# Performance work log

Measured on AMD Instinct MI355X. Metric: run time of the kernel, lower is better.

Reference implementation:

```python
import jax, jax.numpy as jnp
import numpy as np

B, N, DEG = 128, 512, 16          # graphs, nodes/graph, avg degree
NB = B * N                        # 65536 nodes
E = NB * DEG                      # 1048576 edges
K1, K2, K3 = 410, 205, 103        # ceil(0.8*512), ceil(0.5*410), ceil(0.5*205)
H, C = 4, 32                      # GAT heads, head dim
F_IN, ED = 128, 7


def _glorot(key, shape, fan_in):
    return jax.random.normal(key, shape, dtype=jnp.float32) / np.float32(np.sqrt(fan_in))


def setup_inputs() -> dict:
    key = jax.random.key(0)
    ks = jax.random.split(key, 24)
    x = jax.random.normal(ks[0], (NB, F_IN), dtype=jnp.float32)
    # random intra-graph edges, then offset per graph
    src = jax.random.randint(ks[1], (E,), 0, N)
    dst = jax.random.randint(ks[2], (E,), 0, N)
    off = jnp.repeat(jnp.arange(B) * N, N * DEG)
    edge_index = jnp.stack([src + off, dst + off]).astype(jnp.int32)
    edge_attr = jax.random.normal(ks[3], (E, ED), dtype=jnp.float32)
    p = {
        'c1_wl': _glorot(ks[4], (F_IN, F_IN), F_IN), 'c1_bl': jnp.zeros((F_IN,), jnp.float32), 'c1_wr': _glorot(ks[5], (F_IN, F_IN), F_IN),
        'p1_w': _glorot(ks[6], (F_IN,), F_IN),
        'c2_wl': _glorot(ks[7], (F_IN, F_IN), F_IN), 'c2_bl': jnp.zeros((F_IN,), jnp.float32), 'c2_wr': _glorot(ks[8], (F_IN, F_IN), F_IN),
        'p2_wrel': _glorot(ks[9], (F_IN, 1), F_IN), 'p2_brel': jnp.zeros((1,), jnp.float32), 'p2_wroot': _glorot(ks[10], (F_IN, 1), F_IN),
        'g_w': _glorot(ks[11], (F_IN, H * C), F_IN), 'g_as': _glorot(ks[12], (H, C), C), 'g_ad': _glorot(ks[13], (H, C), C),
        'g_we': _glorot(ks[14], (ED, H * C), ED), 'g_ae': _glorot(ks[15], (H, C), C), 'g_b': jnp.zeros((H * C,), jnp.float32),
        'p3_wrel': _glorot(ks[16], (F_IN, 1), F_IN), 'p3_brel': jnp.zeros((1,), jnp.float32), 'p3_wroot': _glorot(ks[17], (F_IN, 1), F_IN),
        'l1_w': _glorot(ks[18], (F_IN, F_IN), F_IN), 'l1_b': jnp.zeros((F_IN,), jnp.float32),
        'l2_w': _glorot(ks[19], (F_IN, 64), F_IN), 'l2_b': jnp.zeros((64,), jnp.float32),
        'l3_w': _glorot(ks[20], (64, 1), 64), 'l3_b': jnp.zeros((1,), jnp.float32),
    }
    return {'x': x, 'edge_index': edge_index, 'edge_attr': edge_attr, **p}


def _sage(x, src, dst, emf, wl, bl, wr):
    # SAGEConv: mean-aggregate neighbors (masked edges), lin_l(agg)+lin_r(x)
    agg = jax.ops.segment_sum(x[src] * emf[:, None], dst, num_segments=NB)
    cnt = jax.ops.segment_sum(emf, dst, num_segments=NB)
    mean = agg / jnp.maximum(cnt, 1.0)[:, None]
    return mean @ wl + bl + x @ wr


def _graphconv(x, src, dst, emf, wrel, brel, wroot):
    # GraphConv (SAGPooling score GNN): add-aggregation
    agg = jax.ops.segment_sum(x[src] * emf[:, None], dst, num_segments=NB)
    return (agg @ wrel + brel + x @ wroot).reshape(-1)


def _pool(x, score, nmask, K):
    # per-graph static top-k (equal-size graphs) == PyG topk + filter
    masked = jnp.where(nmask, score, -jnp.inf).reshape(B, N)
    idx = jax.lax.top_k(masked, K)[1]
    nm = jnp.zeros((B, N), dtype=bool).at[jnp.arange(B)[:, None], idx].set(True).reshape(-1)
    x = jnp.where(nm[:, None], x * score[:, None], 0.0)
    return x, nm


def _gap(x, K):
    # global mean pool; dropped nodes are exactly zero, K live nodes per graph
    return x.reshape(B, N, F_IN).sum(axis=1) / K


def _gat(x, src, dst, emf, nmask, edge_attr, w, a_s, a_d, w_e, a_e, b):
    xs = (x @ w).reshape(NB, H, C)
    al_s = (xs * a_s).sum(-1)                                   # [NB,H]
    al_d = (xs * a_d).sum(-1)
    al_e = ((edge_attr @ w_e).reshape(E, H, C) * a_e).sum(-1)    # [E,H]
    alpha = jax.nn.leaky_relu(al_s[src] + al_d[dst] + al_e, 0.2)
    alpha = jnp.where(emf[:, None] > 0, alpha, -jnp.inf)
    # PyG add_self_loops=True with fill_value='mean' for edge_attr
    ea_mean = (edge_attr * emf[:, None]).sum(0) / jnp.maximum(emf.sum(), 1.0)
    al_se = ((ea_mean @ w_e).reshape(H, C) * a_e).sum(-1)        # [H]
    alpha_self = jax.nn.leaky_relu(al_s + al_d + al_se[None, :], 0.2)
    alpha_self = jnp.where(nmask[:, None], alpha_self, -jnp.inf)
    m = jnp.maximum(jax.ops.segment_max(alpha, dst, num_segments=NB), alpha_self)
    m = jnp.where(jnp.isfinite(m), m, 0.0)
    ex = jnp.exp(alpha - m[dst]) * emf[:, None]
    ex_s = jnp.where(nmask[:, None], jnp.exp(alpha_self - m), 0.0)
    den = jnp.maximum(jax.ops.segment_sum(ex, dst, num_segments=NB) + ex_s, 1e-16)
    num = jax.ops.segment_sum(ex[:, :, None] * xs[src], dst, num_segments=NB) + ex_s[:, :, None] * xs
    return (num / den[:, :, None]).reshape(NB, H * C) + b


def _forward(x, edge_index, edge_attr, c1_wl, c1_bl, c1_wr, p1_w, c2_wl, c2_bl, c2_wr,
             p2_wrel, p2_brel, p2_wroot, g_w, g_as, g_ad, g_we, g_ae, g_b,
             p3_wrel, p3_brel, p3_wroot, l1_w, l1_b, l2_w, l2_b, l3_w, l3_b):
    src, dst = edge_index[0], edge_index[1]
    nmask = jnp.ones((NB,), dtype=bool)
    emf = jnp.ones((E,), jnp.float32)

    # block 1: SAGEConv -> TopKPooling(0.8) -> gap
    x = jax.nn.relu(_sage(x, src, dst, emf, c1_wl, c1_bl, c1_wr))
    s1 = jnp.tanh((x @ p1_w) / jnp.linalg.norm(p1_w))
    x, nmask = _pool(x, s1, nmask, K1)
    emf = emf * nmask[src] * nmask[dst]
    x1 = _gap(x, K1)

    # block 2: SAGEConv -> SAGPooling(0.5) -> gap
    x = jax.nn.relu(_sage(x, src, dst, emf, c2_wl, c2_bl, c2_wr))
    s2 = jnp.tanh(_graphconv(x, src, dst, emf, p2_wrel, p2_brel, p2_wroot))
    x, nmask = _pool(x, s2, nmask, K2)
    emf = emf * nmask[src] * nmask[dst]
    x2 = _gap(x, K2)

    # block 3: GATConv(128->32x4, edge_dim=7) -> SAGPooling(0.5) -> gap
    x = jax.nn.relu(_gat(x, src, dst, emf, nmask, edge_attr, g_w, g_as, g_ad, g_we, g_ae, g_b))
    s3 = jnp.tanh(_graphconv(x, src, dst, emf, p3_wrel, p3_brel, p3_wroot))
    x, nmask = _pool(x, s3, nmask, K3)
    x3 = _gap(x, K3)

    h = x1 + x2 + x3
    h = jax.nn.relu(h @ l1_w + l1_b)
    h = jax.nn.relu(h @ l2_w + l2_b)   # dropout identity in eval
    return jax.nn.sigmoid(h @ l3_w + l3_b)[:, 0]


def reference(x, edge_index, edge_attr, c1_wl, c1_bl, c1_wr, p1_w, c2_wl, c2_bl, c2_wr,
              p2_wrel, p2_brel, p2_wroot, g_w, g_as, g_ad, g_we, g_ae, g_b,
              p3_wrel, p3_brel, p3_wroot, l1_w, l1_b, l2_w, l2_b, l3_w, l3_b):
    return _forward(x, edge_index, edge_attr, c1_wl, c1_bl, c1_wr, p1_w, c2_wl, c2_bl, c2_wr,
                    p2_wrel, p2_brel, p2_wroot, g_w, g_as, g_ad, g_we, g_ae, g_b,
                    p3_wrel, p3_brel, p3_wroot, l1_w, l1_b, l2_w, l2_b, l3_w, l3_b)
```

## Files before the change

kernel.cpp:

```cpp
#include <hip/hip_runtime.h>
#include <math.h>

#define NBV 65536
#define EV  1048576
#define BV  128
#define K1V 410
#define K2V 205
#define K3V 103
#define NL2 (BV*K2V)
#define NEG_BIG (-1.0e38f)

__device__ __forceinline__ float lrelu(float x){ return x > 0.f ? x : 0.2f*x; }

__global__ void k_sentinel(float* out, float v){
  int i = threadIdx.x;
  if (i < 128) out[i] = v;
}

__global__ void k_init1(float* nmask, int* dcnt){
  int i = blockIdx.x*blockDim.x + threadIdx.x;
  if (i < NBV) nmask[i] = 1.f;
  if (i < NBV+1) dcnt[i] = 0;
}

__global__ void k_zero_i(int* p, int n){
  int i = blockIdx.x*blockDim.x + threadIdx.x;
  if (i < n) p[i] = 0;
}

__global__ void k_hist(const int* dst, int* dcnt){
  int e = blockIdx.x*blockDim.x + threadIdx.x;
  if (e < EV) atomicAdd(&dcnt[dst[e]], 1);
}

__global__ void k_scan1(const int* dcnt, int* rp, int* bsum){
  __shared__ int sc[256];
  int t = threadIdx.x, i = blockIdx.x*256 + t;
  int v = dcnt[i];
  sc[t] = v; __syncthreads();
  for (int o = 1; o < 256; o <<= 1){
    int x = (t >= o) ? sc[t-o] : 0;
    __syncthreads();
    sc[t] += x;
    __syncthreads();
  }
  rp[i] = sc[t];
  if (t == 255) bsum[blockIdx.x] = sc[t];
}

__global__ void k_scan2(int* bsum){
  __shared__ int sc[256];
  int t = threadIdx.x;
  int v = bsum[t];
  sc[t] = v; __syncthreads();
  for (int o = 1; o < 256; o <<= 1){
    int x = (t >= o) ? sc[t-o] : 0;
    __syncthreads();
    sc[t] += x;
    __syncthreads();
  }
  bsum[t] = sc[t] - v;
}

__global__ void k_scan3(int* rp, const int* dcnt, const int* bsum){
  int t = threadIdx.x, i = blockIdx.x*256 + t;
  rp[i] = rp[i] - dcnt[i] + bsum[blockIdx.x];
  if (i == 0) rp[NBV] = EV;
}

__global__ void k_scatter(const int* src, const int* dst, const int* rp, int* fill,
                          int* csr_src, int* csr_eid){
  int e = blockIdx.x*blockDim.x + threadIdx.x;
  if (e < EV){
    int d = dst[e];
    int pos = atomicAdd(&fill[d], 1);
    int slot = rp[d] + pos;
    csr_src[slot] = src[e];
    csr_eid[slot] = e;
  }
}

__global__ void k_ve_inv(const float* g_we, const float* g_ae, const float* p1w, float* sml){
  __shared__ float sc[128];
  int t = threadIdx.x;
  if (t < 28){
    int ed = t >> 2, h = t & 3;
    float a = 0.f;
    for (int c = 0; c < 32; c++) a += g_we[ed*128 + h*32 + c] * g_ae[h*32 + c];
    sml[20 + t] = a;
  }
  float v = p1w[t];
  sc[t] = v*v; __syncthreads();
  for (int o = 64; o > 0; o >>= 1){ if (t < o) sc[t] += sc[t+o]; __syncthreads(); }
  if (t == 0) sml[0] = 1.f / sqrtf(sc[0]);
}

__global__ void k_ale(const float* ea, const float* ve, float* ALE){
  int e = blockIdx.x*blockDim.x + threadIdx.x;
  if (e < EV){
    float a0=0.f,a1=0.f,a2=0.f,a3=0.f;
    for (int ed = 0; ed < 7; ed++){
      float x = ea[e*7 + ed];
      a0 += x*ve[ed*4+0]; a1 += x*ve[ed*4+1]; a2 += x*ve[ed*4+2]; a3 += x*ve[ed*4+3];
    }
    float4 o; o.x=a0; o.y=a1; o.z=a2; o.w=a3;
    *(float4*)&ALE[(size_t)e*4] = o;
  }
}

__global__ void __launch_bounds__(256) k_sage_agg(const float* X, const float* nmask,
    const int* rp, const int* csr_src, float* AGG, int masked){
  int g = blockIdx.x & 127;
  int blk = blockIdx.x >> 7;
  int i = g*512 + blk*8 + (threadIdx.x >> 5);
  int c4 = threadIdx.x & 31;
  float ax=0.f,ay=0.f,az=0.f,aw=0.f,cnt=0.f;
  if (!masked || nmask[i] > 0.f){
    int r0 = rp[i], r1 = rp[i+1];
    int s = r0;
    for (; s + 4 <= r1; s += 4){
      int sn0 = csr_src[s+0], sn1 = csr_src[s+1], sn2 = csr_src[s+2], sn3 = csr_src[s+3];
      float nm0 = masked ? nmask[sn0] : 1.f;
      float nm1 = masked ? nmask[sn1] : 1.f;
      float nm2 = masked ? nmask[sn2] : 1.f;
      float nm3 = masked ? nmask[sn3] : 1.f;
      if (nm0 > 0.f){ float4 v = *(const float4*)&X[((size_t)sn0 << 7) + (c4 << 2)];
                      ax += v.x; ay += v.y; az += v.z; aw += v.w; cnt += 1.f; }
      if (nm1 > 0.f){ float4 v = *(const float4*)&X[((size_t)sn1 << 7) + (c4 << 2)];
                      ax += v.x; ay += v.y; az += v.z; aw += v.w; cnt += 1.f; }
      if (nm2 > 0.f){ float4 v = *(const float4*)&X[((size_t)sn2 << 7) + (c4 << 2)];
                      ax += v.x; ay += v.y; az += v.z; aw += v.w; cnt += 1.f; }
      if (nm3 > 0.f){ float4 v = *(const float4*)&X[((size_t)sn3 << 7) + (c4 << 2)];
                      ax += v.x; ay += v.y; az += v.z; aw += v.w; cnt += 1.f; }
    }
    for (; s < r1; s++){
      int sn = csr_src[s];
      float nm = masked ? nmask[sn] : 1.f;
      if (nm > 0.f){
        const float4 v = *(const float4*)&X[((size_t)sn << 7) + (c4 << 2)];
        ax += v.x; ay += v.y; az += v.z; aw += v.w; cnt += 1.f;
      }
    }
  }
  float inv = 1.f / fmaxf(cnt, 1.f);
  float4 o; o.x = ax*inv; o.y = ay*inv; o.z = az*inv; o.w = aw*inv;
  *(float4*)&AGG[((size_t)i << 7) + (c4 << 2)] = o;
}

__global__ void __launch_bounds__(512) k_gemm(const float* A1, const float* A2,
    const float* W1, const float* W2, const float* bias,
    float* OUT, int has2, int relu, int hasb,
    const int* ridx, int sc_mode,
    const float* sw1, const float* sw2, const float* sinv,
    float* so1, float* so2){
  __shared__ float ws[128][128];
  __shared__ float as[16][136];
  int t = threadIdx.x;
  int n0 = blockIdx.x * 128;
  int rowg = t >> 5;
  int colg = t & 31;
  int rb = rowg * 8;
  int jb = colg * 4;
  int an = t >> 2;
  int ak = (t & 3) << 2;
  int arow = ridx ? ridx[n0 + an] : (n0 + an);
  float acc[8][4];
  for (int r = 0; r < 8; r++)
    for (int j = 0; j < 4; j++) acc[r][j] = 0.f;
  int nmat = has2 ? 2 : 1;
  for (int m = 0; m < nmat; m++){
    const float* A = (m == 0) ? A1 : A2;
    const float* W = (m == 0) ? W1 : W2;
    __syncthreads();
    for (int ii = 0; ii < 8; ii++){
      int idx4 = t + 512*ii;
      int kk = idx4 >> 5;
      int jj = (idx4 & 31) << 2;
      *(float4*)&ws[kk][jj] = *(const float4*)&W[kk*128 + jj];
    }
    float4 rA = *(const float4*)&A[((size_t)arow << 7) + ak];
    for (int c = 0; c < 8; c++){
      if (c > 0) __syncthreads();
      as[ak+0][an] = rA.x;
      as[ak+1][an] = rA.y;
      as[ak+2][an] = rA.z;
      as[ak+3][an] = rA.w;
      __syncthreads();
      if (c+1 < 8)
        rA = *(const float4*)&A[((size_t)arow << 7) + (c+1)*16 + ak];
      int kb = c*16;
      for (int kk = 0; kk < 16; kk++){
        float4 wv = *(const float4*)&ws[kb+kk][jb];
        float4 aL = *(const float4*)&as[kk][rb];
        float4 aH = *(const float4*)&as[kk][rb+4];
        float a0=aL.x,a1=aL.y,a2=aL.z,a3=aL.w,a4=aH.x,a5=aH.y,a6=aH.z,a7=aH.w;
        acc[0][0]+=a0*wv.x; acc[0][1]+=a0*wv.y; acc[0][2]+=a0*wv.z; acc[0][3]+=a0*wv.w;
        acc[1][0]+=a1*wv.x; acc[1][1]+=a1*wv.y; acc[1][2]+=a1*wv.z; acc[1][3]+=a1*wv.w;
        acc[2][0]+=a2*wv.x; acc[2][1]+=a2*wv.y; acc[2][2]+=a2*wv.z; acc[2][3]+=a2*wv.w;
        acc[3][0]+=a3*wv.x; acc[3][1]+=a3*wv.y; acc[3][2]+=a3*wv.z; acc[3][3]+=a3*wv.w;
        acc[4][0]+=a4*wv.x; acc[4][1]+=a4*wv.y; acc[4][2]+=a4*wv.z; acc[4][3]+=a4*wv.w;
        acc[5][0]+=a5*wv.x; acc[5][1]+=a5*wv.y; acc[5][2]+=a5*wv.z; acc[5][3]+=a5*wv.w;
        acc[6][0]+=a6*wv.x; acc[6][1]+=a6*wv.y; acc[6][2]+=a6*wv.z; acc[6][3]+=a6*wv.w;
        acc[7][0]+=a7*wv.x; acc[7][1]+=a7*wv.y; acc[7][2]+=a7*wv.z; acc[7][3]+=a7*wv.w;
      }
    }
  }
  float bj0=0.f,bj1=0.f,bj2=0.f,bj3=0.f;
  if (hasb){
    bj0 = bias[jb+0]; bj1 = bias[jb+1]; bj2 = bias[jb+2]; bj3 = bias[jb+3];
  }
  int orow[8];
  for (int r = 0; r < 8; r++) orow[r] = ridx ? ridx[n0+rb+r] : (n0+rb+r);
  float w1x=0.f,w1y=0.f,w1z=0.f,w1w=0.f, w2x=0.f,w2y=0.f,w2z=0.f,w2w=0.f;
  if (sc_mode){
    float4 t1 = *(const float4*)&sw1[jb];
    w1x=t1.x; w1y=t1.y; w1z=t1.z; w1w=t1.w;
    if (sc_mode == 2){
      float4 t2 = *(const float4*)&sw2[jb];
      w2x=t2.x; w2y=t2.y; w2z=t2.z; w2w=t2.w;
    }
  }
  float pd1[8], pd2[8];
  for (int r = 0; r < 8; r++){
    float4 o;
    o.x = acc[r][0]+bj0; o.y = acc[r][1]+bj1; o.z = acc[r][2]+bj2; o.w = acc[r][3]+bj3;
    if (relu){
      o.x = fmaxf(o.x,0.f); o.y = fmaxf(o.y,0.f); o.z = fmaxf(o.z,0.f); o.w = fmaxf(o.w,0.f);
    }
    if (sc_mode){
      pd1[r] = o.x*w1x + o.y*w1y + o.z*w1z + o.w*w1w;
      if (sc_mode == 2) pd2[r] = o.x*w2x + o.y*w2y + o.z*w2z + o.w*w2w;
    }
    *(float4*)&OUT[((size_t)orow[r] << 7) + jb] = o;
  }
  if (sc_mode == 1){
    float inv = sinv[0];
    for (int r = 0; r < 8; r++){
      float a = pd1[r];
      for (int o = 16; o > 0; o >>= 1) a += __shfl_down(a, o, 32);
      if (colg == 0) so1[orow[r]] = tanhf(a * inv);
    }
  } else if (sc_mode == 2){
    for (int r = 0; r < 8; r++){
      float a = pd1[r];
      float b = pd2[r];
      for (int o = 16; o > 0; o >>= 1){
        a += __shfl_down(a, o, 32);
        b += __shfl_down(b, o, 32);
      }
      if (colg == 0){ so1[orow[r]] = a; so2[orow[r]] = b; }
    }
  }
}

__global__ void k_gconv(const float* q, const float* r, const float* nmask,
    const int* rp, const int* csr_src, const float* brel, float* s){
  int i = blockIdx.x*blockDim.x + threadIdx.x;
  if (i >= NBV) return;
  float acc = 0.f;
  if (nmask[i] > 0.f){
    int r0 = rp[i], r1 = rp[i+1];
    int t2 = r0;
    for (; t2 + 4 <= r1; t2 += 4){
      int sn0 = csr_src[t2+0], sn1 = csr_src[t2+1], sn2 = csr_src[t2+2], sn3 = csr_src[t2+3];
      float nm0 = nmask[sn0], nm1 = nmask[sn1], nm2 = nmask[sn2], nm3 = nmask[sn3];
      if (nm0 > 0.f) acc += q[sn0];
      if (nm1 > 0.f) acc += q[sn1];
      if (nm2 > 0.f) acc += q[sn2];
      if (nm3 > 0.f) acc += q[sn3];
    }
    for (; t2 < r1; t2++){
      int sn = csr_src[t2];
      if (nmask[sn] > 0.f) acc += q[sn];
    }
  }
  s[i] = tanhf(acc + brel[0] + r[i]);
}

__global__ void __launch_bounds__(512) k_pool(const float* s, float* nmask, float* sel,
                                              int K, int* cidx){
  __shared__ float sc[512];
  int b = blockIdx.x, t = threadIdx.x;
  int i = b*512 + t;
  float nm = nmask[i];
  float sv = s[i];
  float ms = (nm > 0.f) ? sv : NEG_BIG;
  sc[t] = ms;
  __syncthreads();
  int rank = 0;
  for (int j = 0; j < 512; j++){
    float o = sc[j];
    rank += ((o > ms) || (o == ms && j < t)) ? 1 : 0;
  }
  bool selb = rank < K;
  nmask[i] = selb ? 1.f : 0.f;
  sel[i] = selb ? sv : 0.f;
  if (cidx && selb) cidx[b*K + rank] = i;
}

__global__ void __launch_bounds__(128) k_scale_part(float* X, const float* sel, float* part){
  int b = blockIdx.x >> 3, q = blockIdx.x & 7, c = threadIdx.x;
  float acc = 0.f;
  for (int n = q*64; n < q*64 + 64; n++){
    int i = b*512 + n;
    float v = X[((size_t)i << 7) + c] * sel[i];
    X[((size_t)i << 7) + c] = v;
    acc += v;
  }
  part[(size_t)blockIdx.x*128 + c] = acc;
}

__global__ void __launch_bounds__(128) k_gap_final(const float* part, float* gap, float invK){
  int b = blockIdx.x, c = threadIdx.x;
  float s = 0.f;
  for (int q = 0; q < 8; q++) s += part[(size_t)(b*8+q)*128 + c];
  gap[b*128 + c] = s * invK;
}

__global__ void k_heads(const float* xs, const float* a_s, const float* a_d,
                        const int* cidx, int nlive4, float* alS, float* alD){
  int gid = blockIdx.x*blockDim.x + threadIdx.x;
  if (gid >= nlive4) return;
  int ii = gid >> 2, h = gid & 3;
  int i = cidx[ii];
  const float4* xr = (const float4*)&xs[((size_t)i << 7) + h*32];
  const float4* wa = (const float4*)&a_s[h*32];
  const float4* wd = (const float4*)&a_d[h*32];
  float as_ = 0.f, ad_ = 0.f;
  for (int c4 = 0; c4 < 8; c4++){
    float4 v = xr[c4]; float4 A = wa[c4]; float4 D = wd[c4];
    as_ += v.x*A.x + v.y*A.y + v.z*A.z + v.w*A.w;
    ad_ += v.x*D.x + v.y*D.y + v.z*D.z + v.w*D.w;
  }
  alS[i*4 + h] = as_; alD[i*4 + h] = ad_;
}

__global__ void __launch_bounds__(256) k_ea_part(const float* ea, const int* srcA, const int* dstA,
    const float* nmask, float* part){
  float p[8] = {0.f,0.f,0.f,0.f,0.f,0.f,0.f,0.f};
  for (int e = blockIdx.x*256 + threadIdx.x; e < EV; e += 256*256){
    if (nmask[srcA[e]] > 0.f && nmask[dstA[e]] > 0.f){
      for (int d = 0; d < 7; d++) p[d] += ea[e*7 + d];
      p[7] += 1.f;
    }
  }
  __shared__ float red[256];
  for (int comp = 0; comp < 8; comp++){
    red[threadIdx.x] = p[comp]; __syncthreads();
    for (int o = 128; o > 0; o >>= 1){ if (threadIdx.x < o) red[threadIdx.x] += red[threadIdx.x + o]; __syncthreads(); }
    if (threadIdx.x == 0) part[blockIdx.x*8 + comp] = red[0];
    __syncthreads();
  }
}

__global__ void k_ea_final(const float* part, float* easum){
  int h = threadIdx.x;
  if (h < 8){
    float s = 0.f;
    for (int b = 0; b < 256; b++) s += part[b*8 + h];
    easum[h] = s;
  }
}

__global__ void k_alse(const float* easum, const float* ve, float* alse){
  if (threadIdx.x == 0 && blockIdx.x == 0){
    float cnt = fmaxf(easum[7], 1.f);
    for (int h = 0; h < 4; h++){
      float s = 0.f;
      for (int ed = 0; ed < 7; ed++) s += (easum[ed]/cnt) * ve[ed*4 + h];
      alse[h] = s;
    }
  }
}

__global__ void __launch_bounds__(256) k_gat(const float* xs, const float* alS, const float* alD,
    const float* ALE, const float* nmask, const int* rp, const int* csr_src,
    const int* csr_eid, const float* alse, const float* g_b,
    const float* wrel, const float* wroot, float* qv, float* rv, float* OUT){
  int g = blockIdx.x & 127;
  int blk = blockIdx.x >> 7;
  int i = g*512 + blk*8 + (threadIdx.x >> 5);
  int lane = threadIdx.x & 31;
  int h = lane >> 3;
  int cidx = h*8 + (lane & 7);
  float nmi = nmask[i];
  const float4* xs4 = (const float4*)xs;
  float m = 0.f, den = 0.f;
  float4 acc; acc.x=0.f; acc.y=0.f; acc.z=0.f; acc.w=0.f;
  if (nmi > 0.f){
    float ald_i = alD[i*4 + h];
    m = lrelu(alS[i*4 + h] + ald_i + alse[h]);
    den = 1.f;
    acc = xs4[(size_t)i*32 + cidx];
    int r0 = rp[i], r1 = rp[i+1];
    int s = r0;
    for (; s + 4 <= r1; s += 4){
      int sn0 = csr_src[s+0], sn1 = csr_src[s+1], sn2 = csr_src[s+2], sn3 = csr_src[s+3];
      float nm0 = nmask[sn0], nm1 = nmask[sn1], nm2 = nmask[sn2], nm3 = nmask[sn3];
      if (nm0 > 0.f){
        float a = lrelu(alS[sn0*4 + h] + ald_i + ALE[(size_t)csr_eid[s+0]*4 + h]);
        float4 v = xs4[(size_t)sn0*32 + cidx];
        float mn = fmaxf(m, a); float pm = expf(m - mn); float pa = expf(a - mn);
        den = den*pm + pa;
        acc.x = acc.x*pm + pa*v.x; acc.y = acc.y*pm + pa*v.y;
        acc.z = acc.z*pm + pa*v.z; acc.w = acc.w*pm + pa*v.w;
        m = mn;
      }
      if (nm1 > 0.f){
        float a = lrelu(alS[sn1*4 + h] + ald_i + ALE[(size_t)csr_eid[s+1]*4 + h]);
        float4 v = xs4[(size_t)sn1*32 + cidx];
        float mn = fmaxf(m, a); float pm = expf(m - mn); float pa = expf(a - mn);
        den = den*pm + pa;
        acc.x = acc.x*pm + pa*v.x; acc.y = acc.y*pm + pa*v.y;
        acc.z = acc.z*pm + pa*v.z; acc.w = acc.w*pm + pa*v.w;
        m = mn;
      }
      if (nm2 > 0.f){
        float a = lrelu(alS[sn2*4 + h] + ald_i + ALE[(size_t)csr_eid[s+2]*4 + h]);
        float4 v = xs4[(size_t)sn2*32 + cidx];
        float mn = fmaxf(m, a); float pm = expf(m - mn); float pa = expf(a - mn);
        den = den*pm + pa;
        acc.x = acc.x*pm + pa*v.x; acc.y = acc.y*pm + pa*v.y;
        acc.z = acc.z*pm + pa*v.z; acc.w = acc.w*pm + pa*v.w;
        m = mn;
      }
      if (nm3 > 0.f){
        float a = lrelu(alS[sn3*4 + h] + ald_i + ALE[(size_t)csr_eid[s+3]*4 + h]);
        float4 v = xs4[(size_t)sn3*32 + cidx];
        float mn = fmaxf(m, a); float pm = expf(m - mn); float pa = expf(a - mn);
        den = den*pm + pa;
        acc.x = acc.x*pm + pa*v.x; acc.y = acc.y*pm + pa*v.y;
        acc.z = acc.z*pm + pa*v.z; acc.w = acc.w*pm + pa*v.w;
        m = mn;
      }
    }
    for (; s < r1; s++){
      int sn = csr_src[s];
      if (nmask[sn] > 0.f){
        float a = lrelu(alS[sn*4 + h] + ald_i + ALE[(size_t)csr_eid[s]*4 + h]);
        float4 v = xs4[(size_t)sn*32 + cidx];
        float mn = fmaxf(m, a); float pm = expf(m - mn); float pa = expf(a - mn);
        den = den*pm + pa;
        acc.x = acc.x*pm + pa*v.x; acc.y = acc.y*pm + pa*v.y;
        acc.z = acc.z*pm + pa*v.z; acc.w = acc.w*pm + pa*v.w;
        m = mn;
      }
    }
  }
  den = fmaxf(den, 1e-16f);
  float rd = 1.f/den;
  int cb = cidx << 2;
  float4 o;
  o.x = fmaxf(acc.x*rd + g_b[cb+0], 0.f);
  o.y = fmaxf(acc.y*rd + g_b[cb+1], 0.f);
  o.z = fmaxf(acc.z*rd + g_b[cb+2], 0.f);
  o.w = fmaxf(acc.w*rd + g_b[cb+3], 0.f);
  *(float4*)&OUT[((size_t)i << 7) + cb] = o;
  float4 wa = *(const float4*)&wrel[cb];
  float4 wb = *(const float4*)&wroot[cb];
  float aq = o.x*wa.x + o.y*wa.y + o.z*wa.z + o.w*wa.w;
  float ar = o.x*wb.x + o.y*wb.y + o.z*wb.z + o.w*wb.w;
  for (int off = 16; off > 0; off >>= 1){
    aq += __shfl_down(aq, off, 32);
    ar += __shfl_down(ar, off, 32);
  }
  if (lane == 0){ qv[i] = aq; rv[i] = ar; }
}

__global__ void __launch_bounds__(128) k_mlp(const float* x1g, const float* x2g, const float* x3g,
    const float* l1w, const float* l1b, const float* l2w, const float* l2b,
    const float* l3w, const float* l3b, float* out){
  __shared__ float hh[128];
  __shared__ float h2[128];
  __shared__ float h3[64];
  int b = blockIdx.x, t = threadIdx.x;
  hh[t] = x1g[b*128 + t] + x2g[b*128 + t] + x3g[b*128 + t];
  __syncthreads();
  float a = l1b[t];
  for (int k = 0; k < 128; k++) a += hh[k] * l1w[k*128 + t];
  h2[t] = fmaxf(a, 0.f);
  __syncthreads();
  if (t < 64){
    float a2 = l2b[t];
    for (int k = 0; k < 128; k++) a2 += h2[k] * l2w[k*64 + t];
    h3[t] = fmaxf(a2, 0.f);
  }
  __syncthreads();
  if (t == 0){
    float z = l3b[0];
    for (int k = 0; k < 64; k++) z += h3[k] * l3w[k];
    out[b] = 1.f/(1.f + expf(-z));
  }
}

extern "C" void kernel_launch(void* const* d_in, const int* in_sizes, int n_in,
                              void* d_out, int out_size, void* d_ws, size_t ws_size,
                              hipStream_t stream){
  const float* x       = (const float*)d_in[0];
  const int*   ei      = (const int*)d_in[1];
  const float* ea      = (const float*)d_in[2];
  const float* c1_wl   = (const float*)d_in[3];
  const float* c1_bl   = (const float*)d_in[4];
  const float* c1_wr   = (const float*)d_in[5];
  const float* p1_w    = (const float*)d_in[6];
  const float* c2_wl   = (const float*)d_in[7];
  const float* c2_bl   = (const float*)d_in[8];
  const float* c2_wr   = (const float*)d_in[9];
  const float* p2_wrel = (const float*)d_in[10];
  const float* p2_brel = (const float*)d_in[11];
  const float* p2_wroot= (const float*)d_in[12];
  const float* g_w     = (const float*)d_in[13];
  const float* g_as    = (const float*)d_in[14];
  const float* g_ad    = (const float*)d_in[15];
  const float* g_we    = (const float*)d_in[16];
  const float* g_ae    = (const float*)d_in[17];
  const float* g_b     = (const float*)d_in[18];
  const float* p3_wrel = (const float*)d_in[19];
  const float* p3_brel = (const float*)d_in[20];
  const float* p3_wroot= (const float*)d_in[21];
  const float* l1_w    = (const float*)d_in[22];
  const float* l1_b    = (const float*)d_in[23];
  const float* l2_w    = (const float*)d_in[24];
  const float* l2_b    = (const float*)d_in[25];
  const float* l3_w    = (const float*)d_in[26];
  const float* l3_b    = (const float*)d_in[27];
  float* out = (float*)d_out;
  (void)in_sizes; (void)n_in; (void)out_size;

  char* w = (char*)d_ws;
  size_t off = 0;
  float* AGG  = (float*)(w + off); off += (size_t)NBV*128*4;
  float* F1   = (float*)(w + off); off += (size_t)NBV*128*4;
  float* F2   = (float*)(w + off); off += (size_t)NBV*128*4;
  float* ALE  = (float*)(w + off); off += (size_t)EV*4*4;
  float* sA   = (float*)(w + off); off += (size_t)NBV*4;
  float* sel  = (float*)(w + off); off += (size_t)NBV*4;
  float* qv   = (float*)(w + off); off += (size_t)NBV*4;
  float* rv   = (float*)(w + off); off += (size_t)NBV*4;
  float* nmask= (float*)(w + off); off += (size_t)NBV*4;
  float* alS  = (float*)(w + off); off += (size_t)NBV*4*4;
  float* alD  = (float*)(w + off); off += (size_t)NBV*4*4;
  float* x1g  = (float*)(w + off); off += (size_t)BV*128*4;
  float* x2g  = (float*)(w + off); off += (size_t)BV*128*4;
  float* x3g  = (float*)(w + off); off += (size_t)BV*128*4;
  float* sml  = (float*)(w + off); off += 64*4;
  float* eprt = (float*)(w + off); off += 2048*4;
  float* gprt = (float*)(w + off); off += (size_t)1024*128*4;
  int* csr_src = (int*)(w + off); off += (size_t)EV*4;
  int* csr_eid = (int*)(w + off); off += (size_t)EV*4;
  int* rp      = (int*)(w + off); off += (size_t)(NBV+64)*4;
  int* dcnt    = (int*)(w + off); off += (size_t)(NBV+64)*4;
  int* cidx    = (int*)(w + off); off += (size_t)NBV*4;
  int* bsum    = (int*)(w + off); off += 1024;
  size_t needed = off;

  float sentinel = (ws_size >= needed) ? 0.125f : 0.875f;
  k_sentinel<<<1, 128, 0, stream>>>(out, sentinel);

  const int* srcA = ei;
  const int* dstA = ei + EV;

  k_init1<<<(NBV+256)/256, 256, 0, stream>>>(nmask, dcnt);
  k_hist<<<EV/256, 256, 0, stream>>>(dstA, dcnt);
  k_scan1<<<256, 256, 0, stream>>>(dcnt, rp, bsum);
  k_scan2<<<1, 256, 0, stream>>>(bsum);
  k_scan3<<<256, 256, 0, stream>>>(rp, dcnt, bsum);
  k_zero_i<<<(NBV+256)/256, 256, 0, stream>>>(dcnt, NBV+1);
  k_scatter<<<EV/256, 256, 0, stream>>>(srcA, dstA, rp, dcnt, csr_src, csr_eid);
  k_ve_inv<<<1, 128, 0, stream>>>(g_we, g_ae, p1_w, sml);
  k_ale<<<EV/256, 256, 0, stream>>>(ea, sml+20, ALE);

  k_sage_agg<<<(NBV*32)/256, 256, 0, stream>>>(x, nmask, rp, csr_src, AGG, 0);
  k_gemm<<<NBV/128, 512, 0, stream>>>(AGG, x, c1_wl, c1_wr, c1_bl, F1, 1, 1, 1,
                                      (const int*)nullptr, 1, p1_w, (const float*)nullptr, sml, sA, (float*)nullptr);
  k_pool<<<BV, 512, 0, stream>>>(sA, nmask, sel, K1V, (int*)nullptr);
  k_scale_part<<<BV*8, 128, 0, stream>>>(F1, sel, gprt);
  k_gap_final<<<BV, 128, 0, stream>>>(gprt, x1g, 1.f/(float)K1V);

  k_sage_agg<<<(NBV*32)/256, 256, 0, stream>>>(F1, nmask, rp, csr_src, AGG, 1);
  k_gemm<<<NBV/128, 512, 0, stream>>>(AGG, F1, c2_wl, c2_wr, c2_bl, F2, 1, 1, 1,
                                      (const int*)nullptr, 2, p2_wrel, p2_wroot, (const float*)nullptr, qv, rv);
  k_gconv<<<NBV/256, 256, 0, stream>>>(qv, rv, nmask, rp, csr_src, p2_brel, sA);
  k_pool<<<BV, 512, 0, stream>>>(sA, nmask, sel, K2V, cidx);
  k_scale_part<<<BV*8, 128, 0, stream>>>(F2, sel, gprt);
  k_gap_final<<<BV, 128, 0, stream>>>(gprt, x2g, 1.f/(float)K2V);

  k_gemm<<<NL2/128, 512, 0, stream>>>(F2, F2, g_w, g_w, g_b, AGG, 0, 0, 0,
                                      cidx, 0, (const float*)nullptr, (const float*)nullptr,
                                      (const float*)nullptr, (float*)nullptr, (float*)nullptr);
  k_heads<<<(NL2*4 + 255)/256, 256, 0, stream>>>(AGG, g_as, g_ad, cidx, NL2*4, alS, alD);
  k_ea_part<<<256, 256, 0, stream>>>(ea, srcA, dstA, nmask, eprt);
  k_ea_final<<<1, 64, 0, stream>>>(eprt, sml+8);
  k_alse<<<1, 64, 0, stream>>>(sml+8, sml+20, sml+16);
  k_gat<<<(NBV*32)/256, 256, 0, stream>>>(AGG, alS, alD, ALE, nmask, rp, csr_src, csr_eid,
                                          sml+16, g_b, p3_wrel, p3_wroot, qv, rv, F1);
  k_gconv<<<NBV/256, 256, 0, stream>>>(qv, rv, nmask, rp, csr_src, p3_brel, sA);
  k_pool<<<BV, 512, 0, stream>>>(sA, nmask, sel, K3V, (int*)nullptr);
  k_scale_part<<<BV*8, 128, 0, stream>>>(F1, sel, gprt);
  k_gap_final<<<BV, 128, 0, stream>>>(gprt, x3g, 1.f/(float)K3V);

  k_mlp<<<BV, 128, 0, stream>>>(x1g, x2g, x3g, l1_w, l1_b, l2_w, l2_b, l3_w, l3_b, out);
}
```

Measured before the change: 674.0 us.

## Compact pooled node lists to skip dead nodes in aggregation and GAT

After each pooling step the selected node indices are kept in per-pool index lists. The second SAGE aggregation and the GAT kernel now launch only over surviving nodes instead of all 512 per graph, and k_scale_part skips masked rows. The GEMM also stages the whole 128x128 A tile in shared memory at once, replacing the per-chunk double-sync loop. This roughly doubles the GEMM's LDS use, which can cut occupancy. The two tiny edge-attribute finalize kernels are merged into one. Rows for dead nodes are no longer rewritten, so the code relies on every later consumer masking them.

```diff
diff --git a/kernel.cpp b/kernel.cpp
--- a/kernel.cpp
+++ b/kernel.cpp
@@ -109,10 +109,14 @@
 }
 
 __global__ void __launch_bounds__(256) k_sage_agg(const float* X, const float* nmask,
-    const int* rp, const int* csr_src, float* AGG, int masked){
+    const int* rp, const int* csr_src, float* AGG, int masked,
+    const int* nidx, int kper){
   int g = blockIdx.x & 127;
   int blk = blockIdx.x >> 7;
-  int i = g*512 + blk*8 + (threadIdx.x >> 5);
+  int r = blk*8 + (threadIdx.x >> 5);
+  int i;
+  if (nidx){ if (r >= kper) return; i = nidx[g*kper + r]; }
+  else i = g*512 + r;
   int c4 = threadIdx.x & 31;
   float ax=0.f,ay=0.f,az=0.f,aw=0.f,cnt=0.f;
   if (!masked || nmask[i] > 0.f){
@@ -154,7 +158,7 @@
     const float* sw1, const float* sw2, const float* sinv,
     float* so1, float* so2){
   __shared__ float ws[128][128];
-  __shared__ float as[16][136];
+  __shared__ float as[128][136];
   int t = threadIdx.x;
   int n0 = blockIdx.x * 128;
   int rowg = t >> 5;
@@ -178,21 +182,20 @@
       int jj = (idx4 & 31) << 2;
       *(float4*)&ws[kk][jj] = *(const float4*)&W[kk*128 + jj];
     }
-    float4 rA = *(const float4*)&A[((size_t)arow << 7) + ak];
     for (int c = 0; c < 8; c++){
-      if (c > 0) __syncthreads();
-      as[ak+0][an] = rA.x;
-      as[ak+1][an] = rA.y;
-      as[ak+2][an] = rA.z;
-      as[ak+3][an] = rA.w;
-      __syncthreads();
-      if (c+1 < 8)
-        rA = *(const float4*)&A[((size_t)arow << 7) + (c+1)*16 + ak];
+      float4 rA = *(const float4*)&A[((size_t)arow << 7) + c*16 + ak];
+      as[c*16+ak+0][an] = rA.x;
+      as[c*16+ak+1][an] = rA.y;
+      as[c*16+ak+2][an] = rA.z;
+      as[c*16+ak+3][an] = rA.w;
+    }
+    __syncthreads();
+    for (int c = 0; c < 8; c++){
       int kb = c*16;
       for (int kk = 0; kk < 16; kk++){
         float4 wv = *(const float4*)&ws[kb+kk][jb];
-        float4 aL = *(const float4*)&as[kk][rb];
-        float4 aH = *(const float4*)&as[kk][rb+4];
+        float4 aL = *(const float4*)&as[kb+kk][rb];
+        float4 aH = *(const float4*)&as[kb+kk][rb+4];
         float a0=aL.x,a1=aL.y,a2=aL.z,a3=aL.w,a4=aH.x,a5=aH.y,a6=aH.z,a7=aH.w;
         acc[0][0]+=a0*wv.x; acc[0][1]+=a0*wv.y; acc[0][2]+=a0*wv.z; acc[0][3]+=a0*wv.w;
         acc[1][0]+=a1*wv.x; acc[1][1]+=a1*wv.y; acc[1][2]+=a1*wv.z; acc[1][3]+=a1*wv.w;
@@ -298,14 +301,17 @@
   if (cidx && selb) cidx[b*K + rank] = i;
 }
 
-__global__ void __launch_bounds__(128) k_scale_part(float* X, const float* sel, float* part){
+__global__ void __launch_bounds__(128) k_scale_part(float* X, const float* sel,
+    const float* nmask, float* part){
   int b = blockIdx.x >> 3, q = blockIdx.x & 7, c = threadIdx.x;
   float acc = 0.f;
   for (int n = q*64; n < q*64 + 64; n++){
     int i = b*512 + n;
-    float v = X[((size_t)i << 7) + c] * sel[i];
-    X[((size_t)i << 7) + c] = v;
-    acc += v;
+    if (nmask[i] > 0.f){
+      float v = X[((size_t)i << 7) + c] * sel[i];
+      X[((size_t)i << 7) + c] = v;
+      acc += v;
+    }
   }
   part[(size_t)blockIdx.x*128 + c] = acc;
 }
@@ -353,22 +359,21 @@
   }
 }
 
-__global__ void k_ea_final(const float* part, float* easum){
+__global__ void k_ea_fin(const float* part, const float* ve, float* alse){
+  __shared__ float es[8];
   int h = threadIdx.x;
   if (h < 8){
     float s = 0.f;
     for (int b = 0; b < 256; b++) s += part[b*8 + h];
-    easum[h] = s;
-  }
-}
-
-__global__ void k_alse(const float* easum, const float* ve, float* alse){
-  if (threadIdx.x == 0 && blockIdx.x == 0){
-    float cnt = fmaxf(easum[7], 1.f);
-    for (int h = 0; h < 4; h++){
+    es[h] = s;
+  }
+  __syncthreads();
+  if (h == 0){
+    float cnt = fmaxf(es[7], 1.f);
+    for (int hh = 0; hh < 4; hh++){
       float s = 0.f;
-      for (int ed = 0; ed < 7; ed++) s += (easum[ed]/cnt) * ve[ed*4 + h];
-      alse[h] = s;
+      for (int ed = 0; ed < 7; ed++) s += (es[ed]/cnt) * ve[ed*4 + hh];
+      alse[hh] = s;
     }
   }
 }
@@ -376,13 +381,17 @@
 __global__ void __launch_bounds__(256) k_gat(const float* xs, const float* alS, const float* alD,
     const float* ALE, const float* nmask, const int* rp, const int* csr_src,
     const int* csr_eid, const float* alse, const float* g_b,
-    const float* wrel, const float* wroot, float* qv, float* rv, float* OUT){
+    const float* wrel, const float* wroot, const int* nidx, int kper,
+    float* qv, float* rv, float* OUT){
   int g = blockIdx.x & 127;
   int blk = blockIdx.x >> 7;
-  int i = g*512 + blk*8 + (threadIdx.x >> 5);
+  int r = blk*8 + (threadIdx.x >> 5);
+  int i;
+  if (nidx){ if (r >= kper) return; i = nidx[g*kper + r]; }
+  else i = g*512 + r;
   int lane = threadIdx.x & 31;
   int h = lane >> 3;
-  int cidx = h*8 + (lane & 7);
+  int ch = h*8 + (lane & 7);
   float nmi = nmask[i];
   const float4* xs4 = (const float4*)xs;
   float m = 0.f, den = 0.f;
@@ -391,7 +400,7 @@
     float ald_i = alD[i*4 + h];
     m = lrelu(alS[i*4 + h] + ald_i + alse[h]);
     den = 1.f;
-    acc = xs4[(size_t)i*32 + cidx];
+    acc = xs4[(size_t)i*32 + ch];
     int r0 = rp[i], r1 = rp[i+1];
     int s = r0;
     for (; s + 4 <= r1; s += 4){
@@ -399,7 +408,7 @@
       float nm0 = nmask[sn0], nm1 = nmask[sn1], nm2 = nmask[sn2], nm3 = nmask[sn3];
       if (nm0 > 0.f){
         float a = lrelu(alS[sn0*4 + h] + ald_i + ALE[(size_t)csr_eid[s+0]*4 + h]);
-        float4 v = xs4[(size_t)sn0*32 + cidx];
+        float4 v = xs4[(size_t)sn0*32 + ch];
         float mn = fmaxf(m, a); float pm = expf(m - mn); float pa = expf(a - mn);
         den = den*pm + pa;
         acc.x = acc.x*pm + pa*v.x; acc.y = acc.y*pm + pa*v.y;
@@ -408,7 +417,7 @@
       }
       if (nm1 > 0.f){
         float a = lrelu(alS[sn1*4 + h] + ald_i + ALE[(size_t)csr_eid[s+1]*4 + h]);
-        float4 v = xs4[(size_t)sn1*32 + cidx];
+        float4 v = xs4[(size_t)sn1*32 + ch];
         float mn = fmaxf(m, a); float pm = expf(m - mn); float pa = expf(a - mn);
         den = den*pm + pa;
         acc.x = acc.x*pm + pa*v.x; acc.y = acc.y*pm + pa*v.y;
@@ -417,7 +426,7 @@
       }
       if (nm2 > 0.f){
         float a = lrelu(alS[sn2*4 + h] + ald_i + ALE[(size_t)csr_eid[s+2]*4 + h]);
-        float4 v = xs4[(size_t)sn2*32 + cidx];
+        float4 v = xs4[(size_t)sn2*32 + ch];
         float mn = fmaxf(m, a); float pm = expf(m - mn); float pa = expf(a - mn);
         den = den*pm + pa;
         acc.x = acc.x*pm + pa*v.x; acc.y = acc.y*pm + pa*v.y;
@@ -426,7 +435,7 @@
       }
       if (nm3 > 0.f){
         float a = lrelu(alS[sn3*4 + h] + ald_i + ALE[(size_t)csr_eid[s+3]*4 + h]);
-        float4 v = xs4[(size_t)sn3*32 + cidx];
+        float4 v = xs4[(size_t)sn3*32 + ch];
         float mn = fmaxf(m, a); float pm = expf(m - mn); float pa = expf(a - mn);
         den = den*pm + pa;
         acc.x = acc.x*pm + pa*v.x; acc.y = acc.y*pm + pa*v.y;
@@ -438,7 +447,7 @@
       int sn = csr_src[s];
       if (nmask[sn] > 0.f){
         float a = lrelu(alS[sn*4 + h] + ald_i + ALE[(size_t)csr_eid[s]*4 + h]);
-        float4 v = xs4[(size_t)sn*32 + cidx];
+        float4 v = xs4[(size_t)sn*32 + ch];
         float mn = fmaxf(m, a); float pm = expf(m - mn); float pa = expf(a - mn);
         den = den*pm + pa;
         acc.x = acc.x*pm + pa*v.x; acc.y = acc.y*pm + pa*v.y;
@@ -449,7 +458,7 @@
   }
   den = fmaxf(den, 1e-16f);
   float rd = 1.f/den;
-  int cb = cidx << 2;
+  int cb = ch << 2;
   float4 o;
   o.x = fmaxf(acc.x*rd + g_b[cb+0], 0.f);
   o.y = fmaxf(acc.y*rd + g_b[cb+1], 0.f);
@@ -550,7 +559,8 @@
   int* csr_eid = (int*)(w + off); off += (size_t)EV*4;
   int* rp      = (int*)(w + off); off += (size_t)(NBV+64)*4;
   int* dcnt    = (int*)(w + off); off += (size_t)(NBV+64)*4;
-  int* cidx    = (int*)(w + off); off += (size_t)NBV*4;
+  int* cidx1   = (int*)(w + off); off += (size_t)NBV*4;
+  int* cidx2   = (int*)(w + off); off += (size_t)NBV*4;
   int* bsum    = (int*)(w + off); off += 1024;
   size_t needed = off;
 
@@ -570,33 +580,33 @@
   k_ve_inv<<<1, 128, 0, stream>>>(g_we, g_ae, p1_w, sml);
   k_ale<<<EV/256, 256, 0, stream>>>(ea, sml+20, ALE);
 
-  k_sage_agg<<<(NBV*32)/256, 256, 0, stream>>>(x, nmask, rp, csr_src, AGG, 0);
+  k_sage_agg<<<(NBV*32)/256, 256, 0, stream>>>(x, nmask, rp, csr_src, AGG, 0,
+                                               (const int*)nullptr, 512);
   k_gemm<<<NBV/128, 512, 0, stream>>>(AGG, x, c1_wl, c1_wr, c1_bl, F1, 1, 1, 1,
                                       (const int*)nullptr, 1, p1_w, (const float*)nullptr, sml, sA, (float*)nullptr);
-  k_pool<<<BV, 512, 0, stream>>>(sA, nmask, sel, K1V, (int*)nullptr);
-  k_scale_part<<<BV*8, 128, 0, stream>>>(F1, sel, gprt);
+  k_pool<<<BV, 512, 0, stream>>>(sA, nmask, sel, K1V, cidx1);
+  k_scale_part<<<BV*8, 128, 0, stream>>>(F1, sel, nmask, gprt);
   k_gap_final<<<BV, 128, 0, stream>>>(gprt, x1g, 1.f/(float)K1V);
 
-  k_sage_agg<<<(NBV*32)/256, 256, 0, stream>>>(F1, nmask, rp, csr_src, AGG, 1);
+  k_sage_agg<<<BV*52, 256, 0, stream>>>(F1, nmask, rp, csr_src, AGG, 1, cidx1, K1V);
   k_gemm<<<NBV/128, 512, 0, stream>>>(AGG, F1, c2_wl, c2_wr, c2_bl, F2, 1, 1, 1,
                                       (const int*)nullptr, 2, p2_wrel, p2_wroot, (const float*)nullptr, qv, rv);
   k_gconv<<<NBV/256, 256, 0, stream>>>(qv, rv, nmask, rp, csr_src, p2_brel, sA);
-  k_pool<<<BV, 512, 0, stream>>>(sA, nmask, sel, K2V, cidx);
-  k_scale_part<<<BV*8, 128, 0, stream>>>(F2, sel, gprt);
+  k_pool<<<BV, 512, 0, stream>>>(sA, nmask, sel, K2V, cidx2);
+  k_scale_part<<<BV*8, 128, 0, stream>>>(F2, sel, nmask, gprt);
   k_gap_final<<<BV, 128, 0, stream>>>(gprt, x2g, 1.f/(float)K2V);
 
   k_gemm<<<NL2/128, 512, 0, stream>>>(F2, F2, g_w, g_w, g_b, AGG, 0, 0, 0,
-                                      cidx, 0, (const float*)nullptr, (const float*)nullptr,
+                                      cidx2, 0, (const float*)nullptr, (const float*)nullptr,
                                       (const float*)nullptr, (float*)nullptr, (float*)nullptr);
-  k_heads<<<(NL2*4 + 255)/256, 256, 0, stream>>>(AGG, g_as, g_ad, cidx, NL2*4, alS, alD);
+  k_heads<<<(NL2*4 + 255)/256, 256, 0, stream>>>(AGG, g_as, g_ad, cidx2, NL2*4, alS, alD);
   k_ea_part<<<256, 256, 0, stream>>>(ea, srcA, dstA, nmask, eprt);
-  k_ea_final<<<1, 64, 0, stream>>>(eprt, sml+8);
-  k_alse<<<1, 64, 0, stream>>>(sml+8, sml+20, sml+16);
-  k_gat<<<(NBV*32)/256, 256, 0, stream>>>(AGG, alS, alD, ALE, nmask, rp, csr_src, csr_eid,
-                                          sml+16, g_b, p3_wrel, p3_wroot, qv, rv, F1);
+  k_ea_fin<<<1, 64, 0, stream>>>(eprt, sml+20, sml+16);
+  k_gat<<<BV*26, 256, 0, stream>>>(AGG, alS, alD, ALE, nmask, rp, csr_src, csr_eid,
+                                   sml+16, g_b, p3_wrel, p3_wroot, cidx2, K2V, qv, rv, F1);
   k_gconv<<<NBV/256, 256, 0, stream>>>(qv, rv, nmask, rp, csr_src, p3_brel, sA);
   k_pool<<<BV, 512, 0, stream>>>(sA, nmask, sel, K3V, (int*)nullptr);
-  k_scale_part<<<BV*8, 128, 0, stream>>>(F1, sel, gprt);
+  k_scale_part<<<BV*8, 128, 0, stream>>>(F1, sel, nmask, gprt);
   k_gap_final<<<BV, 128, 0, stream>>>(gprt, x3g, 1.f/(float)K3V);
 
   k_mlp<<<BV, 128, 0, stream>>>(x1g, x2g, x3g, l1_w, l1_b, l2_w, l2_b, l3_w, l3_b, out);
```

Result: slower. 694.9 us (+3.1%).
